# Performance work log

Hardware: AMD Instinct MI355X
Metric: run time of the kernel (lower is better)

The kernel has to match this reference:

```python
import jax, jax.numpy as jnp
import numpy as np

LOSS_PF = 6.0  # penalty base from module-level `loss_pf = 6`


def setup_inputs() -> dict:
    key = jax.random.key(0)
    k1, k2 = jax.random.split(key)
    B, N = 65536, 1024  # N must be a power of two (dim = log2(N) bits)
    y_true = jax.random.uniform(k1, (B, N), dtype=jnp.float32)
    target = jax.random.uniform(k2, (B, N), dtype=jnp.float32)
    return {"y_true": y_true, "target": target}


def reference(y_true, target):
    B, N = y_true.shape
    dim = int(np.log2(N))  # number of bits per class index

    # NLL loss on log(probs): target class = argmax of (one-hot-like) target
    t = jnp.argmax(target, axis=1)  # [B] int
    log_p = jnp.log(y_true + 1e-8)
    ce_loss = -jnp.mean(log_p[jnp.arange(B), t])

    # Bit-Hamming penalty. The torch code builds a [B, N, dim] bit comparison
    # tensor; equivalently, error_num[b, c] = popcount(t_b XOR c).
    # Precompute popcount table over all N class indices (small [N, dim] temp).
    pc = jnp.sum((jnp.arange(N)[:, None] >> jnp.arange(dim)[None, :]) & 1, axis=-1)  # [N]
    # weight = loss_pf ** hamming, zeroed where hamming == 0 (matches where(==1, 0, .))
    w_table = jnp.where(pc == 0, 0.0, LOSS_PF ** pc.astype(jnp.float32))  # [N]

    xor = t[:, None] ^ jnp.arange(N)[None, :]  # [B, N] hamming lookup keys
    w = w_table[xor]                           # [B, N] penalty weights
    pt_loss = jnp.sum(w * y_true) / (B * N)

    return ce_loss + pt_loss
```

## Files before the change

### kernel.cpp

```cpp
#include <hip/hip_runtime.h>
#include <math.h>


#define B_ROWS 65536
#define N_COLS 1024
#define WAVES_PER_BLOCK 4
#define ROWS_BLOCKS 2048
#define ROWS_THREADS (WAVES_PER_BLOCK * 64)

__global__ __launch_bounds__(ROWS_THREADS)
void ce_rows_kernel(const float* __restrict__ y_true,
                    const float* __restrict__ target,
                    float* __restrict__ partials) {
    __shared__ float w_lds[16];
    __shared__ float wave_part[WAVES_PER_BLOCK];

    const int tid = threadIdx.x;
    if (tid < 11) {
        float w = 1.0f;
        for (int p = 0; p < tid; ++p) w *= 6.0f;
        w_lds[tid] = (tid == 0) ? 0.0f : w;
    }
    __syncthreads();

    const int lane = tid & 63;
    const int wid  = tid >> 6;
    const int gwave  = blockIdx.x * WAVES_PER_BLOCK + wid;
    const int nwaves = gridDim.x * WAVES_PER_BLOCK;

    const float invB  = 1.0f / (float)B_ROWS;
    const float invBN = 1.0f / ((float)B_ROWS * (float)N_COLS);

    float acc = 0.0f;

    for (int row = gwave; row < B_ROWS; row += nwaves) {
        const float4* trow = (const float4*)(target + (size_t)row * N_COLS);
        float bestv = -1.0f;
        int   besti = 0;
        #pragma unroll
        for (int k = 0; k < 4; ++k) {
            const int j  = lane + 64 * k;
            const float4 v = trow[j];
            const int c0 = j * 4;
            if (v.x > bestv || (v.x == bestv && c0     < besti)) { bestv = v.x; besti = c0;     }
            if (v.y > bestv || (v.y == bestv && c0 + 1 < besti)) { bestv = v.y; besti = c0 + 1; }
            if (v.z > bestv || (v.z == bestv && c0 + 2 < besti)) { bestv = v.z; besti = c0 + 2; }
            if (v.w > bestv || (v.w == bestv && c0 + 3 < besti)) { bestv = v.w; besti = c0 + 3; }
        }
        #pragma unroll
        for (int m = 32; m >= 1; m >>= 1) {
            const float ov = __shfl_xor(bestv, m, 64);
            const int   oi = __shfl_xor(besti, m, 64);
            if (ov > bestv || (ov == bestv && oi < besti)) { bestv = ov; besti = oi; }
        }
        const int t = besti;

        const float4* yrow = (const float4*)(y_true + (size_t)row * N_COLS);
        float pt = 0.0f;
        float yt = 0.0f;
        #pragma unroll
        for (int k = 0; k < 4; ++k) {
            const int j  = lane + 64 * k;
            const float4 v = yrow[j];
            const int c0 = j * 4;
            const float w0 = w_lds[__popc(t ^ c0)];
            const float w1 = w_lds[__popc(t ^ (c0 + 1))];
            const float w2 = w_lds[__popc(t ^ (c0 + 2))];
            const float w3 = w_lds[__popc(t ^ (c0 + 3))];
            pt += w0 * v.x + w1 * v.y + w2 * v.z + w3 * v.w;
            if (t >= c0 && t < c0 + 4) {
                yt = (t == c0) ? v.x : (t == c0 + 1) ? v.y : (t == c0 + 2) ? v.z : v.w;
            }
        }
        #pragma unroll
        for (int m = 32; m >= 1; m >>= 1) {
            pt += __shfl_xor(pt, m, 64);
            yt += __shfl_xor(yt, m, 64);
        }
        acc += -logf(yt + 1e-8f) * invB + pt * invBN;
    }

    if (lane == 0) wave_part[wid] = acc;
    __syncthreads();
    if (tid == 0) {
        float s = 0.0f;
        #pragma unroll
        for (int w = 0; w < WAVES_PER_BLOCK; ++w) s += wave_part[w];
        partials[blockIdx.x] = s;
    }
}

__global__ __launch_bounds__(256)
void ce_reduce_kernel(const float* __restrict__ partials, int n, float* __restrict__ out) {
    __shared__ float s[256];
    const int tid = threadIdx.x;
    float a = 0.0f;
    for (int i = tid; i < n; i += 256) a += partials[i];
    s[tid] = a;
    __syncthreads();
    for (int off = 128; off > 0; off >>= 1) {
        if (tid < off) s[tid] += s[tid + off];
        __syncthreads();
    }
    if (tid == 0) out[0] = s[0];
}

extern "C" void kernel_launch(void* const* d_in, const int* in_sizes, int n_in,
                              void* d_out, int out_size, void* d_ws, size_t ws_size,
                              hipStream_t stream) {
    const float* y_true = (const float*)d_in[0];
    const float* target = (const float*)d_in[1];
    float* out = (float*)d_out;
    float* partials = (float*)d_ws;

    ce_rows_kernel<<<ROWS_BLOCKS, ROWS_THREADS, 0, stream>>>(y_true, target, partials);
    ce_reduce_kernel<<<1, 256, 0, stream>>>(partials, ROWS_BLOCKS, out);
}
```

Before: 116.4 us.

## Process two rows per wave with all loads issued upfront and deferred reductions

Each wave now handles two rows per iteration and issues all sixteen float4 loads for target and y_true before any compute, so more memory requests are in flight and the y_true load no longer waits on the argmax. The per-row shuffle reductions of the penalty sum and the log term are removed. Values accumulate per lane and are reduced once at the end, and the log is computed only by the lane that holds the target element. The within-lane argmax tie-break check is dropped because strict greater-than over ascending indices already keeps the first maximum. Register pressure rises, and the loop assumes B_ROWS divides evenly by twice the wave count.

```diff
diff --git a/kernel.cpp b/kernel.cpp
--- a/kernel.cpp
+++ b/kernel.cpp
@@ -7,6 +7,26 @@
 #define WAVES_PER_BLOCK 4
 #define ROWS_BLOCKS 2048
 #define ROWS_THREADS (WAVES_PER_BLOCK * 64)
+#define NWAVES (ROWS_BLOCKS * WAVES_PER_BLOCK)
+
+__device__ __forceinline__ void amax4(float4 v, int c0, float& bv, int& bi) {
+    if (v.x > bv) { bv = v.x; bi = c0;     }
+    if (v.y > bv) { bv = v.y; bi = c0 + 1; }
+    if (v.z > bv) { bv = v.z; bi = c0 + 2; }
+    if (v.w > bv) { bv = v.w; bi = c0 + 3; }
+}
+
+__device__ __forceinline__ float wsum4(const float* w_lds, float4 v, int x) {
+    return w_lds[__popc(x)]     * v.x + w_lds[__popc(x ^ 1)] * v.y +
+           w_lds[__popc(x ^ 2)] * v.z + w_lds[__popc(x ^ 3)] * v.w;
+}
+
+__device__ __forceinline__ float pick16(float4 v0, float4 v1, float4 v2, float4 v3, int t) {
+    const int k = (t >> 2) >> 6;
+    const int e = t & 3;
+    float4 s = (k & 2) ? ((k & 1) ? v3 : v2) : ((k & 1) ? v1 : v0);
+    return (e & 2) ? ((e & 1) ? s.w : s.z) : ((e & 1) ? s.y : s.x);
+}
 
 __global__ __launch_bounds__(ROWS_THREADS)
 void ce_rows_kernel(const float* __restrict__ y_true,
@@ -16,71 +36,76 @@
     __shared__ float wave_part[WAVES_PER_BLOCK];
 
     const int tid = threadIdx.x;
-    if (tid < 11) {
+    if (tid < 16) {
         float w = 1.0f;
         for (int p = 0; p < tid; ++p) w *= 6.0f;
         w_lds[tid] = (tid == 0) ? 0.0f : w;
     }
     __syncthreads();
 
-    const int lane = tid & 63;
-    const int wid  = tid >> 6;
-    const int gwave  = blockIdx.x * WAVES_PER_BLOCK + wid;
-    const int nwaves = gridDim.x * WAVES_PER_BLOCK;
+    const int lane  = tid & 63;
+    const int wid   = tid >> 6;
+    const int gwave = blockIdx.x * WAVES_PER_BLOCK + wid;
+
+    float acc_pt = 0.0f;
+    float acc_lg = 0.0f;
+
+    for (int base = gwave; base < B_ROWS; base += 2 * NWAVES) {
+        const int rowA = base;
+        const int rowB = base + NWAVES;
+        const float4* tA = (const float4*)(target + (size_t)rowA * N_COLS);
+        const float4* tB = (const float4*)(target + (size_t)rowB * N_COLS);
+        const float4* yA = (const float4*)(y_true + (size_t)rowA * N_COLS);
+        const float4* yB = (const float4*)(y_true + (size_t)rowB * N_COLS);
+
+        float4 ta0 = tA[lane], ta1 = tA[lane + 64], ta2 = tA[lane + 128], ta3 = tA[lane + 192];
+        float4 tb0 = tB[lane], tb1 = tB[lane + 64], tb2 = tB[lane + 128], tb3 = tB[lane + 192];
+        float4 ya0 = yA[lane], ya1 = yA[lane + 64], ya2 = yA[lane + 128], ya3 = yA[lane + 192];
+        float4 yb0 = yB[lane], yb1 = yB[lane + 64], yb2 = yB[lane + 128], yb3 = yB[lane + 192];
+
+        float bvA = -1.0f, bvB = -1.0f;
+        int   biA = 0,     biB = 0;
+        amax4(ta0, 4 * lane,         bvA, biA);
+        amax4(ta1, 4 * (lane + 64),  bvA, biA);
+        amax4(ta2, 4 * (lane + 128), bvA, biA);
+        amax4(ta3, 4 * (lane + 192), bvA, biA);
+        amax4(tb0, 4 * lane,         bvB, biB);
+        amax4(tb1, 4 * (lane + 64),  bvB, biB);
+        amax4(tb2, 4 * (lane + 128), bvB, biB);
+        amax4(tb3, 4 * (lane + 192), bvB, biB);
+
+        #pragma unroll
+        for (int m = 32; m >= 1; m >>= 1) {
+            float ovA = __shfl_xor(bvA, m, 64); int oiA = __shfl_xor(biA, m, 64);
+            if (ovA > bvA || (ovA == bvA && oiA < biA)) { bvA = ovA; biA = oiA; }
+            float ovB = __shfl_xor(bvB, m, 64); int oiB = __shfl_xor(biB, m, 64);
+            if (ovB > bvB || (ovB == bvB && oiB < biB)) { bvB = ovB; biB = oiB; }
+        }
+        const int tAi = biA;
+        const int tBi = biB;
+
+        acc_pt += wsum4(w_lds, ya0, tAi ^ (4 * lane))
+                + wsum4(w_lds, ya1, tAi ^ (4 * (lane + 64)))
+                + wsum4(w_lds, ya2, tAi ^ (4 * (lane + 128)))
+                + wsum4(w_lds, ya3, tAi ^ (4 * (lane + 192)))
+                + wsum4(w_lds, yb0, tBi ^ (4 * lane))
+                + wsum4(w_lds, yb1, tBi ^ (4 * (lane + 64)))
+                + wsum4(w_lds, yb2, tBi ^ (4 * (lane + 128)))
+                + wsum4(w_lds, yb3, tBi ^ (4 * (lane + 192)));
+
+        if (((tAi >> 2) & 63) == lane)
+            acc_lg += logf(pick16(ya0, ya1, ya2, ya3, tAi) + 1e-8f);
+        if (((tBi >> 2) & 63) == lane)
+            acc_lg += logf(pick16(yb0, yb1, yb2, yb3, tBi) + 1e-8f);
+    }
 
     const float invB  = 1.0f / (float)B_ROWS;
     const float invBN = 1.0f / ((float)B_ROWS * (float)N_COLS);
+    float val = acc_pt * invBN - acc_lg * invB;
+    #pragma unroll
+    for (int m = 32; m >= 1; m >>= 1) val += __shfl_xor(val, m, 64);
 
-    float acc = 0.0f;
-
-    for (int row = gwave; row < B_ROWS; row += nwaves) {
-        const float4* trow = (const float4*)(target + (size_t)row * N_COLS);
-        float bestv = -1.0f;
-        int   besti = 0;
-        #pragma unroll
-        for (int k = 0; k < 4; ++k) {
-            const int j  = lane + 64 * k;
-            const float4 v = trow[j];
-            const int c0 = j * 4;
-            if (v.x > bestv || (v.x == bestv && c0     < besti)) { bestv = v.x; besti = c0;     }
-            if (v.y > bestv || (v.y == bestv && c0 + 1 < besti)) { bestv = v.y; besti = c0 + 1; }
-            if (v.z > bestv || (v.z == bestv && c0 + 2 < besti)) { bestv = v.z; besti = c0 + 2; }
-            if (v.w > bestv || (v.w == bestv && c0 + 3 < besti)) { bestv = v.w; besti = c0 + 3; }
-        }
-        #pragma unroll
-        for (int m = 32; m >= 1; m >>= 1) {
-            const float ov = __shfl_xor(bestv, m, 64);
-            const int   oi = __shfl_xor(besti, m, 64);
-            if (ov > bestv || (ov == bestv && oi < besti)) { bestv = ov; besti = oi; }
-        }
-        const int t = besti;
-
-        const float4* yrow = (const float4*)(y_true + (size_t)row * N_COLS);
-        float pt = 0.0f;
-        float yt = 0.0f;
-        #pragma unroll
-        for (int k = 0; k < 4; ++k) {
-            const int j  = lane + 64 * k;
-            const float4 v = yrow[j];
-            const int c0 = j * 4;
-            const float w0 = w_lds[__popc(t ^ c0)];
-            const float w1 = w_lds[__popc(t ^ (c0 + 1))];
-            const float w2 = w_lds[__popc(t ^ (c0 + 2))];
-            const float w3 = w_lds[__popc(t ^ (c0 + 3))];
-            pt += w0 * v.x + w1 * v.y + w2 * v.z + w3 * v.w;
-            if (t >= c0 && t < c0 + 4) {
-                yt = (t == c0) ? v.x : (t == c0 + 1) ? v.y : (t == c0 + 2) ? v.z : v.w;
-            }
-        }
-        #pragma unroll
-        for (int m = 32; m >= 1; m >>= 1) {
-            pt += __shfl_xor(pt, m, 64);
-            yt += __shfl_xor(yt, m, 64);
-        }
-        acc += -logf(yt + 1e-8f) * invB + pt * invBN;
-    }
-
-    if (lane == 0) wave_part[wid] = acc;
+    if (lane == 0) wave_part[wid] = val;
     __syncthreads();
     if (tid == 0) {
         float s = 0.0f;
```

After: 101.3 us (median of 2 runs). -13.0%, faster.

## Batch four rows per wave with hoisted loads and deferred reductions

Applied to the files above, without the earlier changes.

Each wave now handles four rows per iteration, over two fixed iterations. All target and y_true float4 loads for the four rows are issued up front so more memory requests are in flight. The per-row sum reduction is replaced by per-lane accumulation of the penalty and log terms, with a single wave reduction at the end, and the target log-prob is picked only by the owning lane. The cost is many more live registers (32 float4 values), which may lower occupancy. The loop is also hardcoded to the fixed grid and row count.

```diff
diff --git a/kernel.cpp b/kernel.cpp
--- a/kernel.cpp
+++ b/kernel.cpp
@@ -7,6 +7,14 @@
 #define WAVES_PER_BLOCK 4
 #define ROWS_BLOCKS 2048
 #define ROWS_THREADS (WAVES_PER_BLOCK * 64)
+#define NWAVES (ROWS_BLOCKS * WAVES_PER_BLOCK)
+
+__device__ __forceinline__ float pick16(const float4* yr, int t) {
+    const int k = t >> 8;
+    const int e = t & 3;
+    float4 s = (k & 2) ? ((k & 1) ? yr[3] : yr[2]) : ((k & 1) ? yr[1] : yr[0]);
+    return (e & 2) ? ((e & 1) ? s.w : s.z) : ((e & 1) ? s.y : s.x);
+}
 
 __global__ __launch_bounds__(ROWS_THREADS)
 void ce_rows_kernel(const float* __restrict__ y_true,
@@ -16,71 +24,87 @@
     __shared__ float wave_part[WAVES_PER_BLOCK];
 
     const int tid = threadIdx.x;
-    if (tid < 11) {
+    if (tid < 16) {
         float w = 1.0f;
         for (int p = 0; p < tid; ++p) w *= 6.0f;
         w_lds[tid] = (tid == 0) ? 0.0f : w;
     }
     __syncthreads();
 
-    const int lane = tid & 63;
-    const int wid  = tid >> 6;
-    const int gwave  = blockIdx.x * WAVES_PER_BLOCK + wid;
-    const int nwaves = gridDim.x * WAVES_PER_BLOCK;
+    const int lane  = tid & 63;
+    const int wid   = tid >> 6;
+    const int gwave = blockIdx.x * WAVES_PER_BLOCK + wid;
+
+    float acc_pt = 0.0f;
+    float acc_lg = 0.0f;
+
+    #pragma unroll 1
+    for (int it = 0; it < 2; ++it) {
+        const int base = gwave + it * 4 * NWAVES;
+
+        float4 t4[4][4];
+        #pragma unroll
+        for (int r = 0; r < 4; ++r) {
+            const float4* tp = (const float4*)(target + (size_t)(base + r * NWAVES) * N_COLS);
+            #pragma unroll
+            for (int k = 0; k < 4; ++k) t4[r][k] = tp[lane + 64 * k];
+        }
+
+        float bv[4]; int bi[4];
+        #pragma unroll
+        for (int r = 0; r < 4; ++r) {
+            bv[r] = -1.0f; bi[r] = 0;
+            #pragma unroll
+            for (int k = 0; k < 4; ++k) {
+                const int c0 = 4 * (lane + 64 * k);
+                const float4 v = t4[r][k];
+                if (v.x > bv[r]) { bv[r] = v.x; bi[r] = c0;     }
+                if (v.y > bv[r]) { bv[r] = v.y; bi[r] = c0 + 1; }
+                if (v.z > bv[r]) { bv[r] = v.z; bi[r] = c0 + 2; }
+                if (v.w > bv[r]) { bv[r] = v.w; bi[r] = c0 + 3; }
+            }
+        }
+
+        float4 y4[4][4];
+        #pragma unroll
+        for (int r = 0; r < 4; ++r) {
+            const float4* yp = (const float4*)(y_true + (size_t)(base + r * NWAVES) * N_COLS);
+            #pragma unroll
+            for (int k = 0; k < 4; ++k) y4[r][k] = yp[lane + 64 * k];
+        }
+
+        #pragma unroll
+        for (int m = 32; m >= 1; m >>= 1) {
+            #pragma unroll
+            for (int r = 0; r < 4; ++r) {
+                const float ov = __shfl_xor(bv[r], m, 64);
+                const int   oi = __shfl_xor(bi[r], m, 64);
+                if (ov > bv[r] || (ov == bv[r] && oi < bi[r])) { bv[r] = ov; bi[r] = oi; }
+            }
+        }
+
+        #pragma unroll
+        for (int r = 0; r < 4; ++r) {
+            const int t = bi[r];
+            #pragma unroll
+            for (int k = 0; k < 4; ++k) {
+                const int x = t ^ (4 * (lane + 64 * k));
+                const float4 v = y4[r][k];
+                acc_pt += w_lds[__popc(x)]     * v.x + w_lds[__popc(x ^ 1)] * v.y
+                        + w_lds[__popc(x ^ 2)] * v.z + w_lds[__popc(x ^ 3)] * v.w;
+            }
+            if (((t >> 2) & 63) == lane)
+                acc_lg += logf(pick16(y4[r], t) + 1e-8f);
+        }
+    }
 
     const float invB  = 1.0f / (float)B_ROWS;
     const float invBN = 1.0f / ((float)B_ROWS * (float)N_COLS);
+    float val = acc_pt * invBN - acc_lg * invB;
+    #pragma unroll
+    for (int m = 32; m >= 1; m >>= 1) val += __shfl_xor(val, m, 64);
 
-    float acc = 0.0f;
-
-    for (int row = gwave; row < B_ROWS; row += nwaves) {
-        const float4* trow = (const float4*)(target + (size_t)row * N_COLS);
-        float bestv = -1.0f;
-        int   besti = 0;
-        #pragma unroll
-        for (int k = 0; k < 4; ++k) {
-            const int j  = lane + 64 * k;
-            const float4 v = trow[j];
-            const int c0 = j * 4;
-            if (v.x > bestv || (v.x == bestv && c0     < besti)) { bestv = v.x; besti = c0;     }
-            if (v.y > bestv || (v.y == bestv && c0 + 1 < besti)) { bestv = v.y; besti = c0 + 1; }
-            if (v.z > bestv || (v.z == bestv && c0 + 2 < besti)) { bestv = v.z; besti = c0 + 2; }
-            if (v.w > bestv || (v.w == bestv && c0 + 3 < besti)) { bestv = v.w; besti = c0 + 3; }
-        }
-        #pragma unroll
-        for (int m = 32; m >= 1; m >>= 1) {
-            const float ov = __shfl_xor(bestv, m, 64);
-            const int   oi = __shfl_xor(besti, m, 64);
-            if (ov > bestv || (ov == bestv && oi < besti)) { bestv = ov; besti = oi; }
-        }
-        const int t = besti;
-
-        const float4* yrow = (const float4*)(y_true + (size_t)row * N_COLS);
-        float pt = 0.0f;
-        float yt = 0.0f;
-        #pragma unroll
-        for (int k = 0; k < 4; ++k) {
-            const int j  = lane + 64 * k;
-            const float4 v = yrow[j];
-            const int c0 = j * 4;
-            const float w0 = w_lds[__popc(t ^ c0)];
-            const float w1 = w_lds[__popc(t ^ (c0 + 1))];
-            const float w2 = w_lds[__popc(t ^ (c0 + 2))];
-            const float w3 = w_lds[__popc(t ^ (c0 + 3))];
-            pt += w0 * v.x + w1 * v.y + w2 * v.z + w3 * v.w;
-            if (t >= c0 && t < c0 + 4) {
-                yt = (t == c0) ? v.x : (t == c0 + 1) ? v.y : (t == c0 + 2) ? v.z : v.w;
-            }
-        }
-        #pragma unroll
-        for (int m = 32; m >= 1; m >>= 1) {
-            pt += __shfl_xor(pt, m, 64);
-            yt += __shfl_xor(yt, m, 64);
-        }
-        acc += -logf(yt + 1e-8f) * invB + pt * invBN;
-    }
-
-    if (lane == 0) wave_part[wid] = acc;
+    if (lane == 0) wave_part[wid] = val;
     __syncthreads();
     if (tid == 0) {
         float s = 0.0f;
```

Result: slower. 180.6 us (+55.2%).
